# Kernel tuning notes

Measured on AMD Instinct MI355X. Metric: run time of the kernel, lower is better.

The kernel has to match this reference:

```python
import jax, jax.numpy as jnp
import numpy as np

C = 1024
H = 16
K = 2  # num_states
B, N = 4, 4096


def setup_inputs() -> dict:
    key = jax.random.key(0)
    ks_ = jax.random.split(key, 12)
    s = 1.0 / np.sqrt(C)
    inp = {
        "x": jax.random.normal(ks_[0], (B, N, C), dtype=jnp.float32),
        "Wq": jax.random.normal(ks_[1], (C, C), dtype=jnp.float32) * s,
        "bq": jnp.zeros((C,), dtype=jnp.float32),
        "Wk": jax.random.normal(ks_[2], (K, C, C), dtype=jnp.float32) * s,
        "bk": jnp.zeros((K, C), dtype=jnp.float32),
        "Wv": jax.random.normal(ks_[3], (K, C, C), dtype=jnp.float32) * s,
        "bv": jnp.zeros((K, C), dtype=jnp.float32),
        "Wo": jax.random.normal(ks_[4], (C, C), dtype=jnp.float32) * s,
        "bo": jnp.zeros((C,), dtype=jnp.float32),
        "ln_g": jnp.ones((C,), dtype=jnp.float32),
        "ln_b": jnp.zeros((C,), dtype=jnp.float32),
    }
    return inp


def _heads(t):
    # [..., n, (h d)] -> [..., h, n, d]
    shp = t.shape
    d = shp[-1] // H
    t = t.reshape(shp[:-1] + (H, d))
    return jnp.swapaxes(t, -2, -3)


def reference(x, Wq, bq, Wk, bk, Wv, bv, Wo, bo, ln_g, ln_b):
    dtype = x.dtype
    # residual single-layer projections (ResidualMLP with num_layers=-1)
    q = x + jnp.einsum('bnc,cd->bnd', x, Wq) + bq
    ks = x[None] + jnp.einsum('bnc,kcd->kbnd', x, Wk) + bk[:, None, None, :]
    vs = x[None] + jnp.einsum('bnc,kcd->kbnd', x, Wv) + bv[:, None, None, :]
    q = _heads(q)        # [b,h,n,d]
    ks = _heads(ks)      # [k,b,h,n,d]
    vs = _heads(vs)      # [k,b,h,n,d]
    scale = 1.0 / jnp.sqrt(jnp.asarray(N, dtype=jnp.float32))
    ks = ks.astype(jnp.float32) * scale
    vs = vs.astype(jnp.float32) * scale
    # per-state KV outer-products: [k,b,h,d,e]
    states = jnp.einsum('kbhnd,kbhne->kbhde', ks, vs)
    state = jnp.prod(states, axis=0)  # [b,h,d,e]
    out = jnp.einsum('bhnd,bhde->bhne', q.astype(jnp.float32), state)
    out = out.astype(dtype)
    # [b,h,n,d] -> [b,n,(h d)]
    out = jnp.swapaxes(out, 1, 2).reshape(x.shape[0], x.shape[1], C)
    # LayerNorm
    mu = jnp.mean(out, axis=-1, keepdims=True)
    var = jnp.var(out, axis=-1, keepdims=True)
    out = (out - mu) / jnp.sqrt(var + 1e-5) * ln_g + ln_b
    out = jnp.einsum('bnc,cd->bnd', out, Wo) + bo
    return out
```

## Files before the change

kernel.cpp:

```cpp
#include <hip/hip_runtime.h>
#include <hip/hip_bf16.h>

typedef __attribute__((ext_vector_type(8))) short bf16x8;
typedef __attribute__((ext_vector_type(4))) float f32x4;
typedef __attribute__((ext_vector_type(4))) short s16x4;

__device__ __forceinline__ short f2bf(float f) {
  union { float f; unsigned u; } v; v.f = f;
  unsigned r = v.u + 0x7fffu + ((v.u >> 16) & 1u);
  return (short)(r >> 16);
}

__device__ __forceinline__ float bf2f(short s) {
  union { float f; unsigned u; } v; v.u = ((unsigned)(unsigned short)s) << 16;
  return v.f;
}

#define GLD_LDS(g, l) __builtin_amdgcn_global_load_lds( \
    (const __attribute__((address_space(1))) void*)(g), \
    (__attribute__((address_space(3))) void*)(l), 16, 0, 0)

__global__ __launch_bounds__(256)
void convt_k(const float* __restrict__ x, short* __restrict__ xb,
             short* __restrict__ xbT, float* __restrict__ s) {
  __shared__ short tile[64][72];
  __shared__ float red[4][64];
  const int b = blockIdx.z;
  const int n0 = blockIdx.y * 64;
  const int c0 = blockIdx.x * 64;
  const int t = threadIdx.x;
  const int nl = t >> 4;
  const int c4 = (t & 15) << 2;
  const float* xp = x + ((size_t)b * 4096 + n0) * 1024 + c0;
#pragma unroll
  for (int i = 0; i < 4; ++i) {
    const int n = nl + 16 * i;
    const float4 v = *(const float4*)(xp + (size_t)n * 1024 + c4);
    s16x4 o;
    o[0] = f2bf(v.x); o[1] = f2bf(v.y); o[2] = f2bf(v.z); o[3] = f2bf(v.w);
    *(s16x4*)(&xb[((size_t)b * 4096 + n0 + n) * 1024 + c0 + c4]) = o;
    *(s16x4*)(&tile[n][c4]) = o;
  }
  __syncthreads();
  const int cll = t >> 4;
  const int n4 = (t & 15) << 2;
#pragma unroll
  for (int i = 0; i < 4; ++i) {
    const int c = cll + 16 * i;
    s16x4 o;
    o[0] = tile[n4 + 0][c]; o[1] = tile[n4 + 1][c];
    o[2] = tile[n4 + 2][c]; o[3] = tile[n4 + 3][c];
    *(s16x4*)(&xbT[((size_t)b * 1024 + c0 + c) * 4096 + n0 + n4]) = o;
  }
  const int part = t >> 6, col = t & 63;
  float cs = 0.f;
#pragma unroll
  for (int i = 0; i < 16; ++i) cs += bf2f(tile[part * 16 + i][col]);
  red[part][col] = cs;
  __syncthreads();
  if (part == 0)
    atomicAdd(&s[b * 1024 + c0 + col],
              red[0][col] + red[1][col] + red[2][col] + red[3][col]);
}

__global__ void twc_k(const float* __restrict__ Wq, const float* __restrict__ Wk,
                      const float* __restrict__ Wv, const float* __restrict__ Wo,
                      const float* __restrict__ lng, short* __restrict__ dst,
                      short* __restrict__ wqn) {
  __shared__ float tile[32][33];
  const int z = blockIdx.z;
  const float* src = (z == 0) ? Wq
                   : (z == 1) ? Wk
                   : (z == 2) ? (Wk + 1048576)
                   : (z == 3) ? Wv
                   : (z == 4) ? (Wv + 1048576)
                   : Wo;
  short* d = dst + (size_t)z * 1048576;
  const int tx = threadIdx.x, ty = threadIdx.y;
  const int c0 = blockIdx.y * 32, d0 = blockIdx.x * 32;
#pragma unroll
  for (int i = 0; i < 4; ++i) {
    const int cc = c0 + ty + i * 8;
    const float v = src[(size_t)cc * 1024 + d0 + tx];
    tile[ty + i * 8][tx] = v;
    if (z == 0)
      wqn[(size_t)cc * 1024 + d0 + tx] = f2bf(v + (cc == d0 + tx ? 1.0f : 0.0f));
  }
  __syncthreads();
#pragma unroll
  for (int i = 0; i < 4; ++i) {
    const int cc = c0 + tx;
    const int dd = d0 + ty + i * 8;
    float v = tile[tx][ty + i * 8];
    if (z < 5) {
      if (cc == dd) v += 1.0f;
    } else {
      v *= lng[cc];
    }
    d[(size_t)dd * 1024 + cc] = f2bf(v);
  }
}

__global__ __launch_bounds__(256)
void gemv_k(const short* __restrict__ wt, const float* __restrict__ s,
            float* __restrict__ u, float* __restrict__ w) {
  const int z = blockIdx.z, b = blockIdx.y;
  const int lane = threadIdx.x & 63, wid = threadIdx.x >> 6;
  const short* W = wt + ((size_t)(z + 1) << 20);
  const float* sb = s + b * 1024;
  float* outp = (z < 2) ? (u + (z * 4 + b) * 1024) : (w + ((z - 2) * 4 + b) * 1024);
#pragma unroll 1
  for (int it = 0; it < 16; ++it) {
    const int d = blockIdx.x * 64 + wid * 16 + it;
    const short* row = W + (size_t)d * 1024 + lane * 16;
    float acc = 0.f;
#pragma unroll
    for (int j = 0; j < 16; ++j) acc += bf2f(row[j]) * sb[lane * 16 + j];
#pragma unroll
    for (int o = 32; o > 0; o >>= 1) acc += __shfl_down(acc, o);
    if (lane == 0) outp[d] = acc;
  }
}

__global__ __launch_bounds__(256)
void ut_k(const float* __restrict__ Wo, const float* __restrict__ lng,
          const float* __restrict__ lnb, const float* __restrict__ bo,
          float* __restrict__ u, float* __restrict__ t) {
  const int dl = threadIdx.x & 63;
  const int dd = blockIdx.x * 64 + dl;
  const int part = threadIdx.x >> 6;
  float su = 0.f, st = 0.f;
  for (int c = part * 256; c < part * 256 + 256; ++c) {
    const float w = Wo[(size_t)c * 1024 + dd];
    su += lng[c] * w;
    st += lnb[c] * w;
  }
  __shared__ float rs[4][64], rt[4][64];
  rs[part][dl] = su; rt[part][dl] = st;
  __syncthreads();
  if (part == 0) {
    su = rs[0][dl] + rs[1][dl] + rs[2][dl] + rs[3][dl];
    st = rt[0][dl] + rt[1][dl] + rt[2][dl] + rt[3][dl];
    u[dd] = su;
    t[dd] = st + bo[dd];
  }
}

template <int MODE>
__global__ __launch_bounds__(256)
void g128_k(const short* __restrict__ A0, const short* __restrict__ B0,
            const float* __restrict__ cr0, const float* __restrict__ cr1,
            float* __restrict__ musum, float* __restrict__ sqsum,
            short* __restrict__ obf, float* __restrict__ of32) {
  extern __shared__ short lds[];
  const int tid = threadIdx.x, lane = tid & 63, wid = tid >> 6;
  const int wm = (wid >> 1) << 6, wn = (wid & 1) << 6;
  const int lrow = ((lane >> 3) << 1) | ((lane >> 2) & 1);
  const int kc = ((lane & 3) ^ ((lane >> 3) & 3)) << 3;
  const int cl = lane & 15, khi = lane >> 4;

  int bm0, bn0, koff = 0, b = 0, ld;
  const short *Ap, *Bp;
  if constexpr (MODE == 0) {
    const int swz = (blockIdx.x & 7) * 72 + (blockIdx.x >> 3);
    const int panel = swz / 36;
    int uu2 = swz % 36;
    b = panel >> 2;
    const int kz = panel & 3;
    int ti = 0;
    while (uu2 >= 8 - ti) { uu2 -= 8 - ti; ++ti; }
    const int tj = ti + uu2;
    bm0 = ti << 7; bn0 = tj << 7;
    koff = kz << 10; ld = 4096;
    Ap = A0 + ((size_t)b << 22);
    Bp = Ap;
    of32 += ((size_t)((kz << 2) + b) << 20);
  } else if constexpr (MODE == 1) {
    const int swz = (blockIdx.x & 7) * 64 + (blockIdx.x >> 3);
    b = swz >> 7;
    const int tl = swz & 127;
    bm0 = (tl >> 3) << 7; bn0 = (tl & 7) << 7;
    ld = 1024;
    Ap = A0;
    Bp = B0 + ((size_t)b << 20);
    obf += ((size_t)b << 21);
  } else if constexpr (MODE == 2) {
    const int swz = (blockIdx.x & 7) * 128 + (blockIdx.x >> 3);
    b = swz >> 8;
    const int tl = swz & 255;
    bm0 = (tl >> 3) << 7; bn0 = (tl & 7) << 7;
    ld = 1024;
    Ap = A0 + ((size_t)b << 22);
    Bp = B0 + ((size_t)b << 20);
  } else {
    const int swz = (blockIdx.x & 7) * 128 + (blockIdx.x >> 3);
    bm0 = (swz >> 3) << 7; bn0 = (swz & 7) << 7;
    ld = 1024;
    Ap = A0; Bp = B0;
  }

  f32x4 acc[4][4];
#pragma unroll
  for (int i = 0; i < 4; ++i)
#pragma unroll
    for (int j = 0; j < 4; ++j) acc[i][j] = f32x4{0.f, 0.f, 0.f, 0.f};

  auto stage = [&](int buf, int t) {
    const int k0 = koff + (t << 5) + kc;
    short* ab = lds + buf * 8192;
    short* bb = ab + 4096;
#pragma unroll
    for (int c = 0; c < 2; ++c) {
      const int un = wid * 2 + c;
      GLD_LDS(Ap + (size_t)(bm0 + (un << 4) + lrow) * ld + k0, ab + (un << 9));
      GLD_LDS(Bp + (size_t)(bn0 + (un << 4) + lrow) * ld + k0, bb + (un << 9));
    }
  };

  auto compute = [&](int buf) {
    const short* ab = lds + buf * 8192;
    const short* bb = ab + 4096;
    bf16x8 af[4], bfr[4];
#pragma unroll
    for (int i = 0; i < 4; ++i) {
      const int R = wm + (i << 4) + cl;
      af[i] = *(const bf16x8*)(ab + (R << 5) + ((khi ^ ((R >> 1) & 3)) << 3));
    }
#pragma unroll
    for (int j = 0; j < 4; ++j) {
      const int C = wn + (j << 4) + cl;
      bfr[j] = *(const bf16x8*)(bb + (C << 5) + ((khi ^ ((C >> 1) & 3)) << 3));
    }
#pragma unroll
    for (int i = 0; i < 4; ++i)
#pragma unroll
      for (int j = 0; j < 4; ++j)
        acc[i][j] = __builtin_amdgcn_mfma_f32_16x16x32_bf16(af[i], bfr[j], acc[i][j], 0, 0, 0);
  };

  stage(0, 0);
  stage(1, 1);
  asm volatile("s_waitcnt vmcnt(4)" ::: "memory");
  __builtin_amdgcn_s_barrier();
#pragma unroll 1
  for (int t = 0; t < 30; ++t) {
    stage((t + 2) % 3, t + 2);
    compute(t % 3);
    asm volatile("s_waitcnt vmcnt(4)" ::: "memory");
    __builtin_amdgcn_s_barrier();
  }
  compute(0);
  asm volatile("s_waitcnt vmcnt(0)" ::: "memory");
  __builtin_amdgcn_s_barrier();
  compute(1);

  if constexpr (MODE == 0) {
#pragma unroll
    for (int i = 0; i < 4; ++i)
#pragma unroll
      for (int j = 0; j < 4; ++j) {
        const int col = bn0 + wn + (j << 4) + cl;
        const int rowb = bm0 + wm + (i << 4) + (khi << 2);
#pragma unroll
        for (int r = 0; r < 4; ++r)
          of32[(size_t)(rowb + r) * 1024 + col] = acc[i][j][r];
      }
  } else if constexpr (MODE == 1) {
#pragma unroll
    for (int i = 0; i < 4; ++i)
#pragma unroll
      for (int j = 0; j < 4; ++j) {
        const int col = bn0 + wn + (j << 4) + cl;
        const int rowb = bm0 + wm + (i << 4) + (khi << 2);
#pragma unroll
        for (int r = 0; r < 4; ++r)
          obf[(size_t)(rowb + r) * 1024 + col] = f2bf(acc[i][j][r]);
      }
  } else if constexpr (MODE == 2) {
#pragma unroll
    for (int i = 0; i < 4; ++i) {
      const int rowb = bm0 + wm + (i << 4) + (khi << 2);
      s16x4 pk[4];
#pragma unroll
      for (int j = 0; j < 4; ++j) {
        const int col = bn0 + wn + (j << 4) + cl;
        const float rqc = cr0[b * 1024 + col];
#pragma unroll
        for (int r = 0; r < 4; ++r) pk[j][r] = f2bf(acc[i][j][r] + rqc);
#pragma unroll
        for (int r = 0; r < 4; ++r)
          obf[(size_t)(b * 4096 + rowb + r) * 1024 + col] = pk[j][r];
      }
#pragma unroll
      for (int r = 0; r < 4; ++r) {
        float sv = 0.f, sq = 0.f;
#pragma unroll
        for (int j = 0; j < 4; ++j) {
          const float fv = bf2f(pk[j][r]);
          sv += fv; sq += fv * fv;
        }
#pragma unroll
        for (int m = 1; m < 16; m <<= 1) {
          sv += __shfl_xor(sv, m);
          sq += __shfl_xor(sq, m);
        }
        if (cl == 0) {
          atomicAdd(&musum[b * 4096 + rowb + r], sv);
          atomicAdd(&sqsum[b * 4096 + rowb + r], sq);
        }
      }
    }
  } else {
#pragma unroll
    for (int i = 0; i < 4; ++i) {
      const int rowb = bm0 + wm + (i << 4) + (khi << 2);
      const float4 ms = *(const float4*)(musum + rowb);
      const float4 qs = *(const float4*)(sqsum + rowb);
      float mu[4], rs[4];
      mu[0] = ms.x * (1.0f / 1024.0f); mu[1] = ms.y * (1.0f / 1024.0f);
      mu[2] = ms.z * (1.0f / 1024.0f); mu[3] = ms.w * (1.0f / 1024.0f);
      rs[0] = rsqrtf(fmaxf(qs.x * (1.0f / 1024.0f) - mu[0] * mu[0], 0.f) + 1e-5f);
      rs[1] = rsqrtf(fmaxf(qs.y * (1.0f / 1024.0f) - mu[1] * mu[1], 0.f) + 1e-5f);
      rs[2] = rsqrtf(fmaxf(qs.z * (1.0f / 1024.0f) - mu[2] * mu[2], 0.f) + 1e-5f);
      rs[3] = rsqrtf(fmaxf(qs.w * (1.0f / 1024.0f) - mu[3] * mu[3], 0.f) + 1e-5f);
#pragma unroll
      for (int j = 0; j < 4; ++j) {
        const int col = bn0 + wn + (j << 4) + cl;
        const float uc = cr0[col];
        const float tc = cr1[col];
#pragma unroll
        for (int r = 0; r < 4; ++r)
          of32[(size_t)(rowb + r) * 1024 + col] = rs[r] * (acc[i][j][r] - mu[r] * uc) + tc;
      }
    }
  }
}

__global__ __launch_bounds__(256)
void gred_k(const float* __restrict__ Pg, short* __restrict__ G) {
  __shared__ short tile[64][72];
  const int bid = blockIdx.x;
  const int b = bid / 136;
  int u = bid % 136;
  int ti = 0;
  while (u >= 16 - ti) { u -= 16 - ti; ++ti; }
  const int tj = ti + u;
  const int r = threadIdx.x >> 2;
  const int c0 = (threadIdx.x & 3) << 4;
  float acc[16];
#pragma unroll
  for (int q = 0; q < 16; ++q) acc[q] = 0.f;
#pragma unroll
  for (int kz = 0; kz < 4; ++kz) {
    const float* p = Pg + (((size_t)((kz << 2) + b)) << 20)
                   + (size_t)(ti * 64 + r) * 1024 + tj * 64 + c0;
#pragma unroll
    for (int q4 = 0; q4 < 4; ++q4) {
      const float4 v = ((const float4*)p)[q4];
      acc[q4 * 4 + 0] += v.x; acc[q4 * 4 + 1] += v.y;
      acc[q4 * 4 + 2] += v.z; acc[q4 * 4 + 3] += v.w;
    }
  }
  const float sc = 1.0f / 4096.0f;
  short* gb = G + ((size_t)b << 20);
#pragma unroll
  for (int q4 = 0; q4 < 4; ++q4) {
    s16x4 o;
#pragma unroll
    for (int e = 0; e < 4; ++e) {
      o[e] = f2bf(acc[q4 * 4 + e] * sc);
      tile[r][c0 + q4 * 4 + e] = o[e];
    }
    *(s16x4*)(gb + (size_t)(ti * 64 + r) * 1024 + tj * 64 + c0 + q4 * 4) = o;
  }
  __syncthreads();
  if (ti != tj) {
#pragma unroll
    for (int q4 = 0; q4 < 4; ++q4) {
      s16x4 o;
#pragma unroll
      for (int e = 0; e < 4; ++e) o[e] = tile[c0 + q4 * 4 + e][r];
      *(s16x4*)(gb + (size_t)(tj * 64 + r) * 1024 + ti * 64 + c0 + q4 * 4) = o;
    }
  }
}

__global__ __launch_bounds__(256)
void sw_k(const short* __restrict__ wt, const short* __restrict__ Tt,
          const float* __restrict__ u, const float* __restrict__ w,
          const float* __restrict__ bk, const float* __restrict__ bv,
          const short* __restrict__ wqn, const float* __restrict__ bq,
          short* __restrict__ Beff, float* __restrict__ rq) {
  __shared__ short Al[64 * 40];
  __shared__ short Bl[64 * 40];
  __shared__ short S[64][72];
  const int h = blockIdx.x & 15, b = blockIdx.x >> 4;
  const int tid = threadIdx.x, lane = tid & 63, wid = tid >> 6;
  const int srow = tid >> 2, sch = (tid & 3) << 3;
  const int cl = lane & 15, khi = lane >> 4;

  f32x4 acc2[2][4];
#pragma unroll
  for (int k = 0; k < 2; ++k)
#pragma unroll
    for (int j = 0; j < 4; ++j) acc2[k][j] = f32x4{0.f, 0.f, 0.f, 0.f};

#pragma unroll
  for (int k = 0; k < 2; ++k) {
    const short* Ap = wt + ((size_t)(1 + k) << 20) + ((size_t)(h * 64) << 10);
    const short* Bp = Tt + ((size_t)b << 21) + ((size_t)(k * 1024 + h * 64) << 10);
#pragma unroll 1
    for (int ns = 0; ns < 1024; ns += 32) {
      bf16x8 va = *(const bf16x8*)(Ap + ((size_t)srow << 10) + ns + sch);
      bf16x8 vb = *(const bf16x8*)(Bp + ((size_t)srow << 10) + ns + sch);
      __syncthreads();
      *(bf16x8*)(Al + srow * 40 + sch) = va;
      *(bf16x8*)(Bl + srow * 40 + sch) = vb;
      __syncthreads();
      bf16x8 a = *(const bf16x8*)(Al + (wid * 16 + cl) * 40 + (khi << 3));
#pragma unroll
      for (int j = 0; j < 4; ++j) {
        bf16x8 bb = *(const bf16x8*)(Bl + (j * 16 + cl) * 40 + (khi << 3));
        acc2[k][j] = __builtin_amdgcn_mfma_f32_16x16x32_bf16(a, bb, acc2[k][j], 0, 0, 0);
      }
    }
  }

  const int d0 = wid * 16 + (khi << 2);
  const float invN = 1.0f / 4096.0f;
#pragma unroll
  for (int j = 0; j < 4; ++j) {
    const int e = j * 16 + cl;
    s16x4 pk;
#pragma unroll
    for (int r = 0; r < 4; ++r) {
      const int d = d0 + r;
      float m[2];
#pragma unroll
      for (int k = 0; k < 2; ++k) {
        const float bkd = bk[k * 1024 + h * 64 + d];
        const float bve = bv[k * 1024 + h * 64 + e];
        const float ud = u[(k * 4 + b) * 1024 + h * 64 + d];
        const float we = w[(k * 4 + b) * 1024 + h * 64 + e];
        m[k] = acc2[k][j][r] + (ud * bve + bkd * we + 4096.f * bkd * bve) * invN;
      }
      pk[r] = f2bf(m[0] * m[1]);
    }
    *(s16x4*)(&S[e][d0]) = pk;
  }
  __syncthreads();

  if (wid == 0) {
    float acc = 0.f;
#pragma unroll 1
    for (int d = 0; d < 64; ++d) acc += bq[h * 64 + d] * bf2f(S[lane][d]);
    rq[b * 1024 + h * 64 + lane] = acc;
  }
  bf16x8 af[4][2];
#pragma unroll
  for (int mi = 0; mi < 4; ++mi)
#pragma unroll
    for (int kk = 0; kk < 2; ++kk)
      af[mi][kk] = *(const bf16x8*)(&S[mi * 16 + cl][kk * 32 + khi * 8]);
  const short* wq = wqn + h * 64;
  short* bdst = Beff + ((size_t)b << 20) + ((size_t)(h * 64) << 10);
#pragma unroll 1
  for (int nf = 0; nf < 16; ++nf) {
    const int c0 = wid * 256 + nf * 16;
    const bf16x8 bf0 = *(const bf16x8*)(wq + (size_t)(c0 + cl) * 1024 + khi * 8);
    const bf16x8 bf1 = *(const bf16x8*)(wq + (size_t)(c0 + cl) * 1024 + 32 + khi * 8);
    f32x4 a4[4];
#pragma unroll
    for (int mi = 0; mi < 4; ++mi) {
      a4[mi] = f32x4{0.f, 0.f, 0.f, 0.f};
      a4[mi] = __builtin_amdgcn_mfma_f32_16x16x32_bf16(af[mi][0], bf0, a4[mi], 0, 0, 0);
      a4[mi] = __builtin_amdgcn_mfma_f32_16x16x32_bf16(af[mi][1], bf1, a4[mi], 0, 0, 0);
    }
#pragma unroll
    for (int mi = 0; mi < 4; ++mi)
#pragma unroll
      for (int r = 0; r < 4; ++r)
        bdst[(size_t)(mi * 16 + khi * 4 + r) * 1024 + c0 + cl] = f2bf(a4[mi][r]);
  }
}

extern "C" void kernel_launch(void* const* d_in, const int* in_sizes, int n_in,
                              void* d_out, int out_size, void* d_ws, size_t ws_size,
                              hipStream_t stream) {
  const float* x = (const float*)d_in[0];
  const float* Wq = (const float*)d_in[1];
  const float* bq = (const float*)d_in[2];
  const float* Wk = (const float*)d_in[3];
  const float* bk = (const float*)d_in[4];
  const float* Wv = (const float*)d_in[5];
  const float* bv = (const float*)d_in[6];
  const float* Wo = (const float*)d_in[7];
  const float* bo = (const float*)d_in[8];
  const float* lng = (const float*)d_in[9];
  const float* lnb = (const float*)d_in[10];

  char* ws = (char*)d_ws;
  short* xb = (short*)(ws + 0);
  short* wt = (short*)(ws + 33554432);
  short* wqn = (short*)(ws + 46137344);
  short* Beff = (short*)(ws + 48234496);
  float* rq = (float*)(ws + 56623104);
  float* musum = (float*)(ws + 56639488);
  float* sqsum = (float*)(ws + 56705024);
  float* s = (float*)(ws + 56770560);
  float* u = (float*)(ws + 56786944);
  float* w = (float*)(ws + 56819712);
  float* uu = (float*)(ws + 56852480);
  float* tt = (float*)(ws + 56856576);
  short* xbT = (short*)(ws + 79691776);
  short* Gt = (short*)(ws + 113246208);
  short* Tt = (short*)(ws + 121634816);
  float* Pg = (float*)(ws + 143351808);
  short* oat = xbT;

  hipMemsetAsync(musum, 0, 147456, stream);
  convt_k<<<dim3(16, 64, 4), 256, 0, stream>>>(x, xb, xbT, s);
  twc_k<<<dim3(32, 32, 6), dim3(32, 8), 0, stream>>>(Wq, Wk, Wv, Wo, lng, wt, wqn);
  gemv_k<<<dim3(16, 4, 4), 256, 0, stream>>>(wt, s, u, w);
  ut_k<<<16, 256, 0, stream>>>(Wo, lng, lnb, bo, uu, tt);

  g128_k<0><<<576, 256, 49152, stream>>>(xbT, nullptr, nullptr, nullptr,
                                         nullptr, nullptr, nullptr, Pg);
  gred_k<<<544, 256, 0, stream>>>(Pg, Gt);
  g128_k<1><<<512, 256, 49152, stream>>>(wt + 3145728, Gt, nullptr, nullptr,
                                         nullptr, nullptr, Tt, nullptr);
  sw_k<<<64, 256, 0, stream>>>(wt, Tt, u, w, bk, bv, wqn, bq, Beff, rq);

  g128_k<2><<<1024, 256, 49152, stream>>>(xb, Beff, rq, nullptr,
                                          musum, sqsum, oat, nullptr);
  g128_k<3><<<1024, 256, 49152, stream>>>(oat, wt + 5242880, uu, tt,
                                          musum, sqsum, nullptr, (float*)d_out);
}
```

Measured before the change: 295.2 us.

## Compute full Gram tiles, simplify reduction, and use four LDS buffers

The Gram GEMM (mode 0) now computes all 64 tiles per panel instead of only the 36 upper-triangular ones. This drops the triangular index math, and the reduction kernel becomes a flat elementwise sum with no transpose mirroring. The GEMM kernels switch to 4 LDS buffers (64KB) with power-of-two indexing and set launch bounds to 2 blocks per CU. This adds redundant Gram work and more LDS per block, which may reduce occupancy, in exchange for a simpler reduction and a cheaper ring index.

```diff
diff --git a/kernel.cpp b/kernel.cpp
--- a/kernel.cpp
+++ b/kernel.cpp
@@ -147,11 +147,11 @@
 }
 
 template <int MODE>
-__global__ __launch_bounds__(256)
-void g128_k(const short* __restrict__ A0, const short* __restrict__ B0,
-            const float* __restrict__ cr0, const float* __restrict__ cr1,
-            float* __restrict__ musum, float* __restrict__ sqsum,
-            short* __restrict__ obf, float* __restrict__ of32) {
+__global__ __launch_bounds__(256, 2)
+void g4_k(const short* __restrict__ A0, const short* __restrict__ B0,
+          const float* __restrict__ cr0, const float* __restrict__ cr1,
+          float* __restrict__ musum, float* __restrict__ sqsum,
+          short* __restrict__ obf, float* __restrict__ of32) {
   extern __shared__ short lds[];
   const int tid = threadIdx.x, lane = tid & 63, wid = tid >> 6;
   const int wm = (wid >> 1) << 6, wn = (wid & 1) << 6;
@@ -162,15 +162,12 @@
   int bm0, bn0, koff = 0, b = 0, ld;
   const short *Ap, *Bp;
   if constexpr (MODE == 0) {
-    const int swz = (blockIdx.x & 7) * 72 + (blockIdx.x >> 3);
-    const int panel = swz / 36;
-    int uu2 = swz % 36;
+    const int swz = (blockIdx.x & 7) * 128 + (blockIdx.x >> 3);
+    const int panel = swz >> 6;
     b = panel >> 2;
     const int kz = panel & 3;
-    int ti = 0;
-    while (uu2 >= 8 - ti) { uu2 -= 8 - ti; ++ti; }
-    const int tj = ti + uu2;
-    bm0 = ti << 7; bn0 = tj << 7;
+    const int tl = swz & 63;
+    bm0 = (tl >> 3) << 7; bn0 = (tl & 7) << 7;
     koff = kz << 10; ld = 4096;
     Ap = A0 + ((size_t)b << 22);
     Bp = Ap;
@@ -207,7 +204,7 @@
 
   auto stage = [&](int buf, int t) {
     const int k0 = koff + (t << 5) + kc;
-    short* ab = lds + buf * 8192;
+    short* ab = lds + (buf << 13);
     short* bb = ab + 4096;
 #pragma unroll
     for (int c = 0; c < 2; ++c) {
@@ -218,7 +215,7 @@
   };
 
   auto compute = [&](int buf) {
-    const short* ab = lds + buf * 8192;
+    const short* ab = lds + (buf << 13);
     const short* bb = ab + 4096;
     bf16x8 af[4], bfr[4];
 #pragma unroll
@@ -244,15 +241,15 @@
   __builtin_amdgcn_s_barrier();
 #pragma unroll 1
   for (int t = 0; t < 30; ++t) {
-    stage((t + 2) % 3, t + 2);
-    compute(t % 3);
+    stage((t + 2) & 3, t + 2);
+    compute(t & 3);
     asm volatile("s_waitcnt vmcnt(4)" ::: "memory");
     __builtin_amdgcn_s_barrier();
   }
-  compute(0);
+  compute(2);
   asm volatile("s_waitcnt vmcnt(0)" ::: "memory");
   __builtin_amdgcn_s_barrier();
-  compute(1);
+  compute(3);
 
   if constexpr (MODE == 0) {
 #pragma unroll
@@ -337,52 +334,20 @@
 }
 
 __global__ __launch_bounds__(256)
-void gred_k(const float* __restrict__ Pg, short* __restrict__ G) {
-  __shared__ short tile[64][72];
-  const int bid = blockIdx.x;
-  const int b = bid / 136;
-  int u = bid % 136;
-  int ti = 0;
-  while (u >= 16 - ti) { u -= 16 - ti; ++ti; }
-  const int tj = ti + u;
-  const int r = threadIdx.x >> 2;
-  const int c0 = (threadIdx.x & 3) << 4;
-  float acc[16];
-#pragma unroll
-  for (int q = 0; q < 16; ++q) acc[q] = 0.f;
+void greduce_k(const float* __restrict__ Pg, short* __restrict__ G) {
+  const int b = blockIdx.x >> 10;
+  const int local = ((blockIdx.x & 1023) << 10) + (threadIdx.x << 2);
+  float4 a = {0.f, 0.f, 0.f, 0.f};
 #pragma unroll
   for (int kz = 0; kz < 4; ++kz) {
-    const float* p = Pg + (((size_t)((kz << 2) + b)) << 20)
-                   + (size_t)(ti * 64 + r) * 1024 + tj * 64 + c0;
-#pragma unroll
-    for (int q4 = 0; q4 < 4; ++q4) {
-      const float4 v = ((const float4*)p)[q4];
-      acc[q4 * 4 + 0] += v.x; acc[q4 * 4 + 1] += v.y;
-      acc[q4 * 4 + 2] += v.z; acc[q4 * 4 + 3] += v.w;
-    }
+    const float4 v = *(const float4*)(Pg + (((size_t)((kz << 2) + b)) << 20) + local);
+    a.x += v.x; a.y += v.y; a.z += v.z; a.w += v.w;
   }
   const float sc = 1.0f / 4096.0f;
-  short* gb = G + ((size_t)b << 20);
-#pragma unroll
-  for (int q4 = 0; q4 < 4; ++q4) {
-    s16x4 o;
-#pragma unroll
-    for (int e = 0; e < 4; ++e) {
-      o[e] = f2bf(acc[q4 * 4 + e] * sc);
-      tile[r][c0 + q4 * 4 + e] = o[e];
-    }
-    *(s16x4*)(gb + (size_t)(ti * 64 + r) * 1024 + tj * 64 + c0 + q4 * 4) = o;
-  }
-  __syncthreads();
-  if (ti != tj) {
-#pragma unroll
-    for (int q4 = 0; q4 < 4; ++q4) {
-      s16x4 o;
-#pragma unroll
-      for (int e = 0; e < 4; ++e) o[e] = tile[c0 + q4 * 4 + e][r];
-      *(s16x4*)(gb + (size_t)(tj * 64 + r) * 1024 + ti * 64 + c0 + q4 * 4) = o;
-    }
-  }
+  s16x4 o;
+  o[0] = f2bf(a.x * sc); o[1] = f2bf(a.y * sc);
+  o[2] = f2bf(a.z * sc); o[3] = f2bf(a.w * sc);
+  *(s16x4*)(G + ((size_t)b << 20) + local) = o;
 }
 
 __global__ __launch_bounds__(256)
@@ -524,15 +489,15 @@
   gemv_k<<<dim3(16, 4, 4), 256, 0, stream>>>(wt, s, u, w);
   ut_k<<<16, 256, 0, stream>>>(Wo, lng, lnb, bo, uu, tt);
 
-  g128_k<0><<<576, 256, 49152, stream>>>(xbT, nullptr, nullptr, nullptr,
-                                         nullptr, nullptr, nullptr, Pg);
-  gred_k<<<544, 256, 0, stream>>>(Pg, Gt);
-  g128_k<1><<<512, 256, 49152, stream>>>(wt + 3145728, Gt, nullptr, nullptr,
-                                         nullptr, nullptr, Tt, nullptr);
+  g4_k<0><<<1024, 256, 65536, stream>>>(xbT, nullptr, nullptr, nullptr,
+                                        nullptr, nullptr, nullptr, Pg);
+  greduce_k<<<4096, 256, 0, stream>>>(Pg, Gt);
+  g4_k<1><<<512, 256, 65536, stream>>>(wt + 3145728, Gt, nullptr, nullptr,
+                                       nullptr, nullptr, Tt, nullptr);
   sw_k<<<64, 256, 0, stream>>>(wt, Tt, u, w, bk, bv, wqn, bq, Beff, rq);
 
-  g128_k<2><<<1024, 256, 49152, stream>>>(xb, Beff, rq, nullptr,
-                                          musum, sqsum, oat, nullptr);
-  g128_k<3><<<1024, 256, 49152, stream>>>(oat, wt + 5242880, uu, tt,
-                                          musum, sqsum, nullptr, (float*)d_out);
-}
+  g4_k<2><<<1024, 256, 65536, stream>>>(xb, Beff, rq, nullptr,
+                                        musum, sqsum, oat, nullptr);
+  g4_k<3><<<1024, 256, 65536, stream>>>(oat, wt + 5242880, uu, tt,
+                                        musum, sqsum, nullptr, (float*)d_out);
+}
```

New measurement: 288.4 us. 1.02x faster.
